# Kernel optimization log

Hardware: AMD Instinct MI355X
Metric: run time of the kernel (lower is better)

## Reference

```python
import jax, jax.numpy as jnp
import numpy as np

RADIUS = 1.0
BUMP = 32          # config.bump_steps
SCALE = 100.0      # sigmoid sharpness in compute_ecc
G = 32             # num_graphs

N, E, F = 16000, 48000, 32000
DIM, NDIR = 3, 64
HID, NC = 256, 10


def compute_ecc(h, index, lin):
    # h: [M, D]; lin: [BUMP] thresholds; index: [M] graph ids
    # sigmoid(scale * (lin - h)) broadcast -> [M, BUMP, D], segment-sum over M
    ecc = jax.nn.sigmoid(SCALE * (lin[None, :, None] - h[:, None, :]))
    return jax.ops.segment_sum(ecc, index, num_segments=G)  # [G, BUMP, D]


def setup_inputs() -> dict:
    key = jax.random.key(0)
    ks = jax.random.split(key, 12)
    x = jax.random.normal(ks[0], (N, DIM), dtype=jnp.float32)
    node_weights = jax.random.uniform(ks[1], (N,), dtype=jnp.float32)
    edge_weights = jax.random.uniform(ks[2], (E,), dtype=jnp.float32)
    face_weights = jax.random.uniform(ks[3], (F,), dtype=jnp.float32)
    v = jax.random.normal(ks[4], (DIM, NDIR), dtype=jnp.float32)
    v = v / jnp.linalg.norm(v, axis=0, keepdims=True)  # unit directions
    W1 = jax.random.normal(ks[5], (HID, NDIR * BUMP), dtype=jnp.float32) * 0.02
    b1 = jnp.zeros((HID,), dtype=jnp.float32)
    W2 = jax.random.normal(ks[6], (NC, HID), dtype=jnp.float32) * 0.02
    b2 = jnp.zeros((NC,), dtype=jnp.float32)
    edge_index = jax.random.randint(ks[7], (2, E), 0, N, dtype=jnp.int64)
    face = jax.random.randint(ks[8], (3, F), 0, N, dtype=jnp.int64)
    batch_ids = jnp.sort(jax.random.randint(ks[9], (N,), 0, G, dtype=jnp.int64))
    return {"x": x, "node_weights": node_weights, "edge_weights": edge_weights,
            "face_weights": face_weights, "v": v, "W1": W1, "b1": b1,
            "W2": W2, "b2": b2, "edge_index": edge_index, "face": face,
            "batch_ids": batch_ids}


def reference(x, node_weights, edge_weights, face_weights, v, W1, b1, W2, b2,
              edge_index, face, batch_ids):
    lin = jnp.linspace(-RADIUS, RADIUS, BUMP, dtype=jnp.float32)
    # node heights: weighted coords projected onto directions -> [N, D]
    nh = (x * node_weights[:, None]) @ v
    # edge heights: max over the 2 endpoints, then weight -> [E, D]
    eh = jnp.maximum(nh[edge_index[0]], nh[edge_index[1]]) * edge_weights[:, None]
    idx_e = batch_ids[edge_index[0]]
    # face heights: max over the 3 vertices -> [F, D]
    fh = jnp.max(nh[face], axis=0) * face_weights[:, None]
    idx_f = batch_ids[face[0]]
    ecc = compute_ecc(nh, batch_ids, lin)   # [G, BUMP, D]
    ecc = ecc - compute_ecc(eh, idx_e, lin)
    ecc = ecc + compute_ecc(fh, idx_f, lin)
    flat = ecc.reshape(G, -1)               # [G, BUMP*D]
    h = jax.nn.relu(flat @ W1.T + b1)
    logits = h @ W2.T + b2
    return (logits, flat)
```

## Files before the change

kernel.cpp:

```cpp
#include <hip/hip_runtime.h>
#include <hip/hip_bf16.h>

constexpr int NN = 16000, NE = 48000, NF = 32000;
constexpr int ND = 64, NB = 32, NG = 32;
constexpr int HIDN = 256, NCLS = 10;
constexpr int CHB = 32;
constexpr int EFB = (NE + NF + 255) / 256;
constexpr int PREB = (NN * ND) / 256;
constexpr int CAPE = 4096, CAPF = 4096;
constexpr float KLOG = 144.26950408889634f;
constexpr float DLT  = 9.307710457348151f;
constexpr float INV_DLT = 0.10743849569269015f;
constexpr int HBINS = 39;

constexpr int NH_OFF   = 0;
constexpr int ECCF_OFF = NH_OFF + NN * ND;
constexpr int CUR_OFF  = ECCF_OFF + NG * NB * ND;
constexpr int NOFS_OFF = CUR_OFF + 64;
constexpr int PE_OFF   = NOFS_OFF + 34;
constexpr int PF_OFF   = PE_OFF + NG * CAPE / 2;
constexpr int HB_OFF   = PF_OFF + NG * CAPF / 2;
constexpr int ZERO_CNT = NG * NB * ND;

__device__ __forceinline__ int clamp_node(int n) {
    return ((unsigned)n < (unsigned)NN) ? n : 0;
}
template<bool BF> __device__ __forceinline__ float ldf(const void* p, int i) {
    return BF ? __bfloat162float(((const __hip_bfloat16*)p)[i]) : ((const float*)p)[i];
}
template<bool I64> __device__ __forceinline__ int ldi(const int* p, int i) {
    return I64 ? p[2 * i] : p[i];
}

__device__ __forceinline__ bool detect_bf(const void* xp) {
    const unsigned* xw = (const unsigned*)xp;
    unsigned w = xw[threadIdx.x & 63];
    return __ballot(((w >> 23) & 0xFFu) >= 200u) != 0ull;
}
__device__ __forceinline__ bool detect_i64(const int* eip) {
    const unsigned* eiw = (const unsigned*)eip;
    unsigned o = eiw[2 * (threadIdx.x & 63) + 1];
    return __ballot(o != 0u) == 0ull;
}

__device__ __forceinline__ void accum_hist(float h, float s, float* hb) {
    const float KDEC = __builtin_amdgcn_exp2f(-DLT);
    float hkL = fmaf(h, KLOG, KLOG);
    float fl = floorf((hkL - 14.0f) * INV_DLT);
    int jlo = (int)fl + 1;
    if (jlo >= 32) return;
    if (jlo < -4) { hb[4 * 64] += s; return; }
    float t0 = fmaf(-(fl + 1.0f), DLT, hkL);
    float e  = __builtin_amdgcn_exp2f(t0);
    float s0 = __builtin_amdgcn_rcpf(1.0f + e);  e *= KDEC;
    float s1 = __builtin_amdgcn_rcpf(1.0f + e);  e *= KDEC;
    float s2 = __builtin_amdgcn_rcpf(1.0f + e);
    float* p = hb + (jlo + 4) * 64;
    float v0 = p[0], v1 = p[64], v2 = p[128], v3 = p[192];
    p[0]   = v0 + s * s0;
    p[64]  = v1 + s * (s1 - s0);
    p[128] = v2 + s * (s2 - s1);
    p[192] = v3 + s * (1.0f - s2);
}

template<bool BF, bool I64>
__device__ __forceinline__ void pre_body(const void* x, const void* nw, const void* v,
                                         const int* ei, const int* fc, const int* batch,
                                         float* wsf, int* wsi, unsigned* cur,
                                         unsigned short* pe, unsigned short* pf,
                                         unsigned* cnt, unsigned* base) {
    int t = threadIdx.x;
    int gid = blockIdx.x * 256 + t;

    if (gid < ZERO_CNT) wsf[ECCF_OFF + gid] = 0.0f;

    if (gid < NN) {
        int gn = ldi<I64>(batch, gid) & (NG - 1);
        int gp = (gid > 0) ? (ldi<I64>(batch, gid - 1) & (NG - 1)) : -1;
        for (int gg = gp + 1; gg <= gn; gg++) wsi[NOFS_OFF + gg] = gid;
        if (gid == NN - 1)
            for (int gg = gn + 1; gg <= NG; gg++) wsi[NOFS_OFF + gg] = NN;
    }

    {
        int n = gid >> 6, d = gid & 63;
        float h = fmaf(ldf<BF>(x, n*3+2), ldf<BF>(v, 2*ND+d),
                  fmaf(ldf<BF>(x, n*3+1), ldf<BF>(v, ND+d),
                       ldf<BF>(x, n*3+0) * ldf<BF>(v, d))) * ldf<BF>(nw, n);
        wsf[NH_OFF + gid] = h;
    }

    if (blockIdx.x < EFB) {
        if (t < 64) cnt[t] = 0;
        __syncthreads();
        int id = blockIdx.x * 256 + t;
        int bin = 0; unsigned rank = 0; bool act = false;
        if (id < NE + NF) {
            if (id < NE) bin = ldi<I64>(batch, clamp_node(ldi<I64>(ei, id))) & 31;
            else bin = 32 + (ldi<I64>(batch, clamp_node(ldi<I64>(fc, id - NE))) & 31);
            act = true;
            rank = atomicAdd(&cnt[bin], 1u);
        }
        __syncthreads();
        if (t < 64) base[t] = cnt[t] ? atomicAdd(&cur[t], cnt[t]) : 0u;
        __syncthreads();
        if (act) {
            int off = (int)(base[bin] + rank);
            if (bin < 32) { if (off < CAPE) pe[bin * CAPE + off] = (unsigned short)id; }
            else { if (off < CAPF) pf[(bin - 32) * CAPF + off] = (unsigned short)(id - NE); }
        }
    }
}
__global__ __launch_bounds__(256) void k_pre(const void* __restrict__ x,
                                             const void* __restrict__ nw,
                                             const void* __restrict__ v,
                                             const int* __restrict__ ei,
                                             const int* __restrict__ fc,
                                             const int* __restrict__ batch,
                                             float* __restrict__ wsf,
                                             int* __restrict__ wsi,
                                             unsigned* __restrict__ cur,
                                             unsigned short* __restrict__ pe,
                                             unsigned short* __restrict__ pf) {
    __shared__ unsigned cnt[64], base[64];
    bool bf = detect_bf(x), i64 = detect_i64(ei);
    if (bf)  { if (i64) pre_body<true,true >(x,nw,v,ei,fc,batch,wsf,wsi,cur,pe,pf,cnt,base);
               else     pre_body<true,false>(x,nw,v,ei,fc,batch,wsf,wsi,cur,pe,pf,cnt,base); }
    else     { if (i64) pre_body<false,true >(x,nw,v,ei,fc,batch,wsf,wsi,cur,pe,pf,cnt,base);
               else     pre_body<false,false>(x,nw,v,ei,fc,batch,wsf,wsi,cur,pe,pf,cnt,base); }
}

template<bool BF, bool I64>
__device__ __forceinline__ void ecc_body(const int* ei, const int* fc,
                                         const void* ew, const void* fw,
                                         const float* nh, const int* wsi,
                                         const unsigned* cur, float* eccf,
                                         const unsigned short* pe,
                                         const unsigned short* pf,
                                         float* hist) {
    int t = threadIdx.x;
    int d = t & 63;
    int w = __builtin_amdgcn_readfirstlane(t) >> 6;
    int g  = blockIdx.x >> 5;
    int cb = blockIdx.x & (CHB - 1);
    int sid = cb * 4 + w;
    const int S = CHB * 4;

    for (int j = t; j < 4 * HBINS * 64; j += 256) hist[j] = 0.0f;
    __syncthreads();

    float* hb = hist + w * (HBINS * 64) + d;

    int ns = wsi[NOFS_OFF + g], nend = wsi[NOFS_OFF + g + 1];
    int i = ns + sid;
    for (; i + 3 * S < nend; i += 4 * S) {
        float h1 = nh[i * ND + d];
        float h2 = nh[(i + S) * ND + d];
        float h3 = nh[(i + 2 * S) * ND + d];
        float h4 = nh[(i + 3 * S) * ND + d];
        accum_hist(h1, 1.0f, hb);
        accum_hist(h2, 1.0f, hb);
        accum_hist(h3, 1.0f, hb);
        accum_hist(h4, 1.0f, hb);
    }
    for (; i < nend; i += S) accum_hist(nh[i * ND + d], 1.0f, hb);

    int ecnt = min((int)cur[g], CAPE);
    i = sid;
    for (; i + 3 * S < ecnt; i += 4 * S) {
        int e1 = pe[g * CAPE + i];
        int e2 = pe[g * CAPE + i + S];
        int e3 = pe[g * CAPE + i + 2 * S];
        int e4 = pe[g * CAPE + i + 3 * S];
        int a1 = clamp_node(ldi<I64>(ei, e1)), b1 = clamp_node(ldi<I64>(ei, NE + e1));
        int a2 = clamp_node(ldi<I64>(ei, e2)), b2 = clamp_node(ldi<I64>(ei, NE + e2));
        int a3 = clamp_node(ldi<I64>(ei, e3)), b3 = clamp_node(ldi<I64>(ei, NE + e3));
        int a4 = clamp_node(ldi<I64>(ei, e4)), b4 = clamp_node(ldi<I64>(ei, NE + e4));
        float w1 = ldf<BF>(ew, e1), w2 = ldf<BF>(ew, e2);
        float w3 = ldf<BF>(ew, e3), w4 = ldf<BF>(ew, e4);
        float h1 = fmaxf(nh[a1 * ND + d], nh[b1 * ND + d]) * w1;
        float h2 = fmaxf(nh[a2 * ND + d], nh[b2 * ND + d]) * w2;
        float h3 = fmaxf(nh[a3 * ND + d], nh[b3 * ND + d]) * w3;
        float h4 = fmaxf(nh[a4 * ND + d], nh[b4 * ND + d]) * w4;
        accum_hist(h1, -1.0f, hb);
        accum_hist(h2, -1.0f, hb);
        accum_hist(h3, -1.0f, hb);
        accum_hist(h4, -1.0f, hb);
    }
    for (; i < ecnt; i += S) {
        int e = pe[g * CAPE + i];
        int a = clamp_node(ldi<I64>(ei, e)), b = clamp_node(ldi<I64>(ei, NE + e));
        accum_hist(fmaxf(nh[a * ND + d], nh[b * ND + d]) * ldf<BF>(ew, e), -1.0f, hb);
    }

    int fcnt = min((int)cur[32 + g], CAPF);
    i = sid;
    for (; i + 3 * S < fcnt; i += 4 * S) {
        int f1 = pf[g * CAPF + i];
        int f2 = pf[g * CAPF + i + S];
        int f3 = pf[g * CAPF + i + 2 * S];
        int f4 = pf[g * CAPF + i + 3 * S];
        int a1 = clamp_node(ldi<I64>(fc, f1)), b1 = clamp_node(ldi<I64>(fc, NF + f1));
        int c1 = clamp_node(ldi<I64>(fc, 2*NF + f1));
        int a2 = clamp_node(ldi<I64>(fc, f2)), b2 = clamp_node(ldi<I64>(fc, NF + f2));
        int c2 = clamp_node(ldi<I64>(fc, 2*NF + f2));
        int a3 = clamp_node(ldi<I64>(fc, f3)), b3 = clamp_node(ldi<I64>(fc, NF + f3));
        int c3 = clamp_node(ldi<I64>(fc, 2*NF + f3));
        int a4 = clamp_node(ldi<I64>(fc, f4)), b4 = clamp_node(ldi<I64>(fc, NF + f4));
        int c4 = clamp_node(ldi<I64>(fc, 2*NF + f4));
        float w1 = ldf<BF>(fw, f1), w2 = ldf<BF>(fw, f2);
        float w3 = ldf<BF>(fw, f3), w4 = ldf<BF>(fw, f4);
        float h1 = fmaxf(fmaxf(nh[a1*ND+d], nh[b1*ND+d]), nh[c1*ND+d]) * w1;
        float h2 = fmaxf(fmaxf(nh[a2*ND+d], nh[b2*ND+d]), nh[c2*ND+d]) * w2;
        float h3 = fmaxf(fmaxf(nh[a3*ND+d], nh[b3*ND+d]), nh[c3*ND+d]) * w3;
        float h4 = fmaxf(fmaxf(nh[a4*ND+d], nh[b4*ND+d]), nh[c4*ND+d]) * w4;
        accum_hist(h1, 1.0f, hb);
        accum_hist(h2, 1.0f, hb);
        accum_hist(h3, 1.0f, hb);
        accum_hist(h4, 1.0f, hb);
    }
    for (; i < fcnt; i += S) {
        int f = pf[g * CAPF + i];
        int a = clamp_node(ldi<I64>(fc, f)), b = clamp_node(ldi<I64>(fc, NF + f));
        int c = clamp_node(ldi<I64>(fc, 2*NF + f));
        accum_hist(fmaxf(fmaxf(nh[a*ND+d], nh[b*ND+d]), nh[c*ND+d]) * ldf<BF>(fw, f),
                   1.0f, hb);
    }

    __syncthreads();
    for (int o = t; o < HBINS * 64; o += 256)
        hist[o] += hist[HBINS*64 + o] + hist[2*HBINS*64 + o] + hist[3*HBINS*64 + o];
    __syncthreads();
    if (t < 64) {
        float run = hist[t] + hist[64 + t] + hist[128 + t] + hist[192 + t];
        float* eb = eccf + g * (NB * ND) + t;
        for (int j = 0; j < 32; j++) {
            run += hist[(j + 4) * 64 + t];
            atomicAdd(eb + j * 64, run);
        }
    }
}
__global__ __launch_bounds__(256, 4) void k_ecc(const int* __restrict__ ei,
                                                const int* __restrict__ fc,
                                                const void* __restrict__ ew,
                                                const void* __restrict__ fw,
                                                const float* __restrict__ nh,
                                                const int* __restrict__ wsi,
                                                const unsigned* __restrict__ cur,
                                                float* __restrict__ eccf,
                                                const unsigned short* __restrict__ pe,
                                                const unsigned short* __restrict__ pf,
                                                const void* __restrict__ x) {
    __shared__ float hist[4 * HBINS * 64];
    bool bf = detect_bf(x), i64 = detect_i64(ei);
    if (bf)  { if (i64) ecc_body<true,true >(ei,fc,ew,fw,nh,wsi,cur,eccf,pe,pf,hist);
               else     ecc_body<true,false>(ei,fc,ew,fw,nh,wsi,cur,eccf,pe,pf,hist); }
    else     { if (i64) ecc_body<false,true >(ei,fc,ew,fw,nh,wsi,cur,eccf,pe,pf,hist);
               else     ecc_body<false,false>(ei,fc,ew,fw,nh,wsi,cur,eccf,pe,pf,hist); }
}

template<bool BF>
__device__ __forceinline__ void mlp1_body(const void* W1, const void* b1,
                                          const float* eccf, float* hbuf,
                                          void* outv, float* red, float* pr) {
    int g = blockIdx.x >> 3, hc = blockIdx.x & 7;
    int t = threadIdx.x;

    const float4* fp = (const float4*)(eccf + g * (NB * ND) + t * 8);
    float4 fa = fp[0], fb = fp[1];
    float fl[8] = {fa.x, fa.y, fa.z, fa.w, fb.x, fb.y, fb.z, fb.w};

    if (hc == 0) {
        int ob = NG * NCLS + g * (NB * ND) + t * 8;
        if (BF) {
#pragma unroll
            for (int j = 0; j < 8; j++)
                ((__hip_bfloat16*)outv)[ob + j] = __float2bfloat16(fl[j]);
        } else {
            ((float4*)((float*)outv + ob))[0] = fa;
            ((float4*)((float*)outv + ob))[1] = fb;
        }
    }

    float acc[32];
#pragma unroll
    for (int r = 0; r < 32; r++) acc[r] = 0.0f;
#pragma unroll 4
    for (int r = 0; r < 32; r++) {
        size_t wb = (size_t)(hc * 32 + r) * (NB * ND) + t * 8;
        float wv[8];
        if (BF) {
            uint4 u = *(const uint4*)((const __hip_bfloat16*)W1 + wb);
            wv[0] = __uint_as_float(u.x << 16); wv[1] = __uint_as_float(u.x & 0xffff0000u);
            wv[2] = __uint_as_float(u.y << 16); wv[3] = __uint_as_float(u.y & 0xffff0000u);
            wv[4] = __uint_as_float(u.z << 16); wv[5] = __uint_as_float(u.z & 0xffff0000u);
            wv[6] = __uint_as_float(u.w << 16); wv[7] = __uint_as_float(u.w & 0xffff0000u);
        } else {
            float4 a = *(const float4*)((const float*)W1 + wb);
            float4 b = *(const float4*)((const float*)W1 + wb + 4);
            wv[0]=a.x; wv[1]=a.y; wv[2]=a.z; wv[3]=a.w;
            wv[4]=b.x; wv[5]=b.y; wv[6]=b.z; wv[7]=b.w;
        }
        float s = 0.0f;
#pragma unroll
        for (int j = 0; j < 8; j++) s = fmaf(wv[j], fl[j], s);
        acc[r] = s;
    }

#pragma unroll
    for (int r = 0; r < 32; r++) red[t * 33 + r] = acc[r];
    __syncthreads();
    {
        int r = t >> 3, s8 = t & 7;
        float sum = 0.0f;
#pragma unroll
        for (int i = 0; i < 32; i++) sum += red[(s8 * 32 + i) * 33 + r];
        pr[r * 8 + s8] = sum;
    }
    __syncthreads();
    if (t < 32) {
        float h = ldf<BF>(b1, hc * 32 + t);
#pragma unroll
        for (int s8 = 0; s8 < 8; s8++) h += pr[t * 8 + s8];
        hbuf[g * HIDN + hc * 32 + t] = fmaxf(h, 0.0f);
    }
}
__global__ __launch_bounds__(256) void k_mlp1(const void* __restrict__ W1,
                                              const void* __restrict__ b1,
                                              const float* __restrict__ eccf,
                                              float* __restrict__ hbuf,
                                              void* __restrict__ outv,
                                              const void* __restrict__ x) {
    __shared__ float red[256 * 33];
    __shared__ float pr[256];
    if (detect_bf(x)) mlp1_body<true>(W1, b1, eccf, hbuf, outv, red, pr);
    else              mlp1_body<false>(W1, b1, eccf, hbuf, outv, red, pr);
}

template<bool BF>
__device__ __forceinline__ void mlp2_body(const void* W2, const void* b2,
                                          const float* hbuf, void* outv, float* hs) {
    int g = blockIdx.x, t = threadIdx.x;
    hs[t] = hbuf[g * HIDN + t];
    __syncthreads();
    int w = t >> 6, lane = t & 63;
    for (int c = w; c < NCLS; c += 4) {
        float p = hs[lane]        * ldf<BF>(W2, c * HIDN + lane)
                + hs[lane + 64]   * ldf<BF>(W2, c * HIDN + lane + 64)
                + hs[lane + 128]  * ldf<BF>(W2, c * HIDN + lane + 128)
                + hs[lane + 192]  * ldf<BF>(W2, c * HIDN + lane + 192);
#pragma unroll
        for (int off = 32; off >= 1; off >>= 1) p += __shfl_xor(p, off);
        if (lane == 0) {
            float r = p + ldf<BF>(b2, c);
            if (BF) ((__hip_bfloat16*)outv)[g * NCLS + c] = __float2bfloat16(r);
            else    ((float*)outv)[g * NCLS + c] = r;
        }
    }
}
__global__ __launch_bounds__(256) void k_mlp2(const void* __restrict__ W2,
                                              const void* __restrict__ b2,
                                              const float* __restrict__ hbuf,
                                              void* __restrict__ outv,
                                              const void* __restrict__ x) {
    __shared__ float hs[HIDN];
    if (detect_bf(x)) mlp2_body<true>(W2, b2, hbuf, outv, hs);
    else              mlp2_body<false>(W2, b2, hbuf, outv, hs);
}

extern "C" void kernel_launch(void* const* d_in, const int* in_sizes, int n_in,
                              void* d_out, int out_size, void* d_ws, size_t ws_size,
                              hipStream_t stream) {
    const void* x  = d_in[0];
    const void* nw = d_in[1];
    const void* ew = d_in[2];
    const void* fw = d_in[3];
    const void* v  = d_in[4];
    const void* W1 = d_in[5];
    const void* b1 = d_in[6];
    const void* W2 = d_in[7];
    const void* b2 = d_in[8];
    const int* ei    = (const int*)d_in[9];
    const int* fc    = (const int*)d_in[10];
    const int* batch = (const int*)d_in[11];

    float*    wsf = (float*)d_ws;
    unsigned* wsu = (unsigned*)d_ws;
    int*      wsi = (int*)d_ws;
    float*    nh   = wsf + NH_OFF;
    float*    eccf = wsf + ECCF_OFF;
    unsigned* cur  = wsu + CUR_OFF;
    float*    hbuf = wsf + HB_OFF;
    unsigned short* pe = (unsigned short*)(wsi + PE_OFF);
    unsigned short* pf = (unsigned short*)(wsi + PF_OFF);

    hipMemsetAsync((char*)d_ws + (size_t)CUR_OFF * 4, 0, 64 * 4, stream);

    k_pre<<<PREB, 256, 0, stream>>>(x, nw, v, ei, fc, batch, wsf, wsi, cur, pe, pf);
    k_ecc<<<NG * CHB, 256, 0, stream>>>(ei, fc, ew, fw, nh, wsi, cur, eccf, pe, pf, x);
    k_mlp1<<<NG * 8, 256, 0, stream>>>(W1, b1, eccf, hbuf, d_out, x);
    k_mlp2<<<NG, 256, 0, stream>>>(W2, b2, hbuf, d_out, x);
}
```

Before: 124.5 us.

## Pack edge/face endpoints and weights into records during bucketing, prefetch in ecc

The bucketing pass now writes compact per-graph records holding packed endpoint indices and the weight, instead of 16-bit edge/face ids. The ECC kernel then reads one record per edge or face rather than chasing ids into the edge_index, face and weight arrays, which removes one level of dependent gathers. The unrolled loops also software-prefetch the next batch of records while the current node heights are being loaded. The cost is larger workspace records and extra gathers in the pre kernel. The 14-bit index packing holds because node ids are below 16384.

Result: faster. 121.1 us (-2.7%).

```diff
diff --git a/kernel.cpp b/kernel.cpp
--- a/kernel.cpp
+++ b/kernel.cpp
@@ -13,13 +13,16 @@
 constexpr float INV_DLT = 0.10743849569269015f;
 constexpr int HBINS = 39;
 
+struct alignas(8)  ERec { unsigned ab; float w; };
+struct alignas(16) FRec { unsigned ab; unsigned c; float w; unsigned pad; };
+
 constexpr int NH_OFF   = 0;
 constexpr int ECCF_OFF = NH_OFF + NN * ND;
 constexpr int CUR_OFF  = ECCF_OFF + NG * NB * ND;
 constexpr int NOFS_OFF = CUR_OFF + 64;
-constexpr int PE_OFF   = NOFS_OFF + 34;
-constexpr int PF_OFF   = PE_OFF + NG * CAPE / 2;
-constexpr int HB_OFF   = PF_OFF + NG * CAPF / 2;
+constexpr int ER_OFF   = NOFS_OFF + 36;
+constexpr int FR_OFF   = ER_OFF + NG * CAPE * 2;
+constexpr int HB_OFF   = FR_OFF + NG * CAPF * 4;
 constexpr int ZERO_CNT = NG * NB * ND;
 
 __device__ __forceinline__ int clamp_node(int n) {
@@ -66,8 +69,9 @@
 template<bool BF, bool I64>
 __device__ __forceinline__ void pre_body(const void* x, const void* nw, const void* v,
                                          const int* ei, const int* fc, const int* batch,
+                                         const void* ew, const void* fw,
                                          float* wsf, int* wsi, unsigned* cur,
-                                         unsigned short* pe, unsigned short* pf,
+                                         ERec* er, FRec* fr,
                                          unsigned* cnt, unsigned* base) {
     int t = threadIdx.x;
     int gid = blockIdx.x * 256 + t;
@@ -106,8 +110,24 @@
         __syncthreads();
         if (act) {
             int off = (int)(base[bin] + rank);
-            if (bin < 32) { if (off < CAPE) pe[bin * CAPE + off] = (unsigned short)id; }
-            else { if (off < CAPF) pf[(bin - 32) * CAPF + off] = (unsigned short)(id - NE); }
+            if (bin < 32) {
+                if (off < CAPE) {
+                    unsigned a = (unsigned)clamp_node(ldi<I64>(ei, id));
+                    unsigned b = (unsigned)clamp_node(ldi<I64>(ei, NE + id));
+                    ERec r; r.ab = a | (b << 14); r.w = ldf<BF>(ew, id);
+                    er[bin * CAPE + off] = r;
+                }
+            } else {
+                if (off < CAPF) {
+                    int fid = id - NE;
+                    unsigned a = (unsigned)clamp_node(ldi<I64>(fc, fid));
+                    unsigned b = (unsigned)clamp_node(ldi<I64>(fc, NF + fid));
+                    unsigned c = (unsigned)clamp_node(ldi<I64>(fc, 2 * NF + fid));
+                    FRec r; r.ab = a | (b << 14); r.c = c;
+                    r.w = ldf<BF>(fw, fid); r.pad = 0u;
+                    fr[(bin - 32) * CAPF + off] = r;
+                }
+            }
         }
     }
 }
@@ -117,27 +137,28 @@
                                              const int* __restrict__ ei,
                                              const int* __restrict__ fc,
                                              const int* __restrict__ batch,
+                                             const void* __restrict__ ew,
+                                             const void* __restrict__ fw,
                                              float* __restrict__ wsf,
                                              int* __restrict__ wsi,
                                              unsigned* __restrict__ cur,
-                                             unsigned short* __restrict__ pe,
-                                             unsigned short* __restrict__ pf) {
+                                             ERec* __restrict__ er,
+                                             FRec* __restrict__ fr) {
     __shared__ unsigned cnt[64], base[64];
     bool bf = detect_bf(x), i64 = detect_i64(ei);
-    if (bf)  { if (i64) pre_body<true,true >(x,nw,v,ei,fc,batch,wsf,wsi,cur,pe,pf,cnt,base);
-               else     pre_body<true,false>(x,nw,v,ei,fc,batch,wsf,wsi,cur,pe,pf,cnt,base); }
-    else     { if (i64) pre_body<false,true >(x,nw,v,ei,fc,batch,wsf,wsi,cur,pe,pf,cnt,base);
-               else     pre_body<false,false>(x,nw,v,ei,fc,batch,wsf,wsi,cur,pe,pf,cnt,base); }
-}
-
-template<bool BF, bool I64>
-__device__ __forceinline__ void ecc_body(const int* ei, const int* fc,
-                                         const void* ew, const void* fw,
-                                         const float* nh, const int* wsi,
-                                         const unsigned* cur, float* eccf,
-                                         const unsigned short* pe,
-                                         const unsigned short* pf,
-                                         float* hist) {
+    if (bf)  { if (i64) pre_body<true,true >(x,nw,v,ei,fc,batch,ew,fw,wsf,wsi,cur,er,fr,cnt,base);
+               else     pre_body<true,false>(x,nw,v,ei,fc,batch,ew,fw,wsf,wsi,cur,er,fr,cnt,base); }
+    else     { if (i64) pre_body<false,true >(x,nw,v,ei,fc,batch,ew,fw,wsf,wsi,cur,er,fr,cnt,base);
+               else     pre_body<false,false>(x,nw,v,ei,fc,batch,ew,fw,wsf,wsi,cur,er,fr,cnt,base); }
+}
+
+__global__ __launch_bounds__(256, 4) void k_ecc(const float* __restrict__ nh,
+                                                const int* __restrict__ wsi,
+                                                const unsigned* __restrict__ cur,
+                                                float* __restrict__ eccf,
+                                                const ERec* __restrict__ er,
+                                                const FRec* __restrict__ fr) {
+    __shared__ float hist[4 * HBINS * 64];
     int t = threadIdx.x;
     int d = t & 63;
     int w = __builtin_amdgcn_readfirstlane(t) >> 6;
@@ -166,65 +187,66 @@
     for (; i < nend; i += S) accum_hist(nh[i * ND + d], 1.0f, hb);
 
     int ecnt = min((int)cur[g], CAPE);
+    const ERec* eg = er + g * CAPE;
     i = sid;
-    for (; i + 3 * S < ecnt; i += 4 * S) {
-        int e1 = pe[g * CAPE + i];
-        int e2 = pe[g * CAPE + i + S];
-        int e3 = pe[g * CAPE + i + 2 * S];
-        int e4 = pe[g * CAPE + i + 3 * S];
-        int a1 = clamp_node(ldi<I64>(ei, e1)), b1 = clamp_node(ldi<I64>(ei, NE + e1));
-        int a2 = clamp_node(ldi<I64>(ei, e2)), b2 = clamp_node(ldi<I64>(ei, NE + e2));
-        int a3 = clamp_node(ldi<I64>(ei, e3)), b3 = clamp_node(ldi<I64>(ei, NE + e3));
-        int a4 = clamp_node(ldi<I64>(ei, e4)), b4 = clamp_node(ldi<I64>(ei, NE + e4));
-        float w1 = ldf<BF>(ew, e1), w2 = ldf<BF>(ew, e2);
-        float w3 = ldf<BF>(ew, e3), w4 = ldf<BF>(ew, e4);
-        float h1 = fmaxf(nh[a1 * ND + d], nh[b1 * ND + d]) * w1;
-        float h2 = fmaxf(nh[a2 * ND + d], nh[b2 * ND + d]) * w2;
-        float h3 = fmaxf(nh[a3 * ND + d], nh[b3 * ND + d]) * w3;
-        float h4 = fmaxf(nh[a4 * ND + d], nh[b4 * ND + d]) * w4;
-        accum_hist(h1, -1.0f, hb);
-        accum_hist(h2, -1.0f, hb);
-        accum_hist(h3, -1.0f, hb);
-        accum_hist(h4, -1.0f, hb);
+    if (i + 3 * S < ecnt) {
+        ERec r1 = eg[i], r2 = eg[i + S], r3 = eg[i + 2 * S], r4 = eg[i + 3 * S];
+        for (;;) {
+            int ni = i + 4 * S;
+            bool more = (ni + 3 * S < ecnt);
+            float a1 = nh[(r1.ab & 16383) * ND + d], b1 = nh[((r1.ab >> 14) & 16383) * ND + d];
+            float a2 = nh[(r2.ab & 16383) * ND + d], b2 = nh[((r2.ab >> 14) & 16383) * ND + d];
+            float a3 = nh[(r3.ab & 16383) * ND + d], b3 = nh[((r3.ab >> 14) & 16383) * ND + d];
+            float a4 = nh[(r4.ab & 16383) * ND + d], b4 = nh[((r4.ab >> 14) & 16383) * ND + d];
+            ERec n1, n2, n3, n4;
+            if (more) { n1 = eg[ni]; n2 = eg[ni + S]; n3 = eg[ni + 2 * S]; n4 = eg[ni + 3 * S]; }
+            accum_hist(fmaxf(a1, b1) * r1.w, -1.0f, hb);
+            accum_hist(fmaxf(a2, b2) * r2.w, -1.0f, hb);
+            accum_hist(fmaxf(a3, b3) * r3.w, -1.0f, hb);
+            accum_hist(fmaxf(a4, b4) * r4.w, -1.0f, hb);
+            i = ni;
+            if (!more) break;
+            r1 = n1; r2 = n2; r3 = n3; r4 = n4;
+        }
     }
     for (; i < ecnt; i += S) {
-        int e = pe[g * CAPE + i];
-        int a = clamp_node(ldi<I64>(ei, e)), b = clamp_node(ldi<I64>(ei, NE + e));
-        accum_hist(fmaxf(nh[a * ND + d], nh[b * ND + d]) * ldf<BF>(ew, e), -1.0f, hb);
+        ERec r = eg[i];
+        float ha = nh[(r.ab & 16383) * ND + d], hbv = nh[((r.ab >> 14) & 16383) * ND + d];
+        accum_hist(fmaxf(ha, hbv) * r.w, -1.0f, hb);
     }
 
     int fcnt = min((int)cur[32 + g], CAPF);
+    const FRec* fg = fr + g * CAPF;
     i = sid;
-    for (; i + 3 * S < fcnt; i += 4 * S) {
-        int f1 = pf[g * CAPF + i];
-        int f2 = pf[g * CAPF + i + S];
-        int f3 = pf[g * CAPF + i + 2 * S];
-        int f4 = pf[g * CAPF + i + 3 * S];
-        int a1 = clamp_node(ldi<I64>(fc, f1)), b1 = clamp_node(ldi<I64>(fc, NF + f1));
-        int c1 = clamp_node(ldi<I64>(fc, 2*NF + f1));
-        int a2 = clamp_node(ldi<I64>(fc, f2)), b2 = clamp_node(ldi<I64>(fc, NF + f2));
-        int c2 = clamp_node(ldi<I64>(fc, 2*NF + f2));
-        int a3 = clamp_node(ldi<I64>(fc, f3)), b3 = clamp_node(ldi<I64>(fc, NF + f3));
-        int c3 = clamp_node(ldi<I64>(fc, 2*NF + f3));
-        int a4 = clamp_node(ldi<I64>(fc, f4)), b4 = clamp_node(ldi<I64>(fc, NF + f4));
-        int c4 = clamp_node(ldi<I64>(fc, 2*NF + f4));
-        float w1 = ldf<BF>(fw, f1), w2 = ldf<BF>(fw, f2);
-        float w3 = ldf<BF>(fw, f3), w4 = ldf<BF>(fw, f4);
-        float h1 = fmaxf(fmaxf(nh[a1*ND+d], nh[b1*ND+d]), nh[c1*ND+d]) * w1;
-        float h2 = fmaxf(fmaxf(nh[a2*ND+d], nh[b2*ND+d]), nh[c2*ND+d]) * w2;
-        float h3 = fmaxf(fmaxf(nh[a3*ND+d], nh[b3*ND+d]), nh[c3*ND+d]) * w3;
-        float h4 = fmaxf(fmaxf(nh[a4*ND+d], nh[b4*ND+d]), nh[c4*ND+d]) * w4;
-        accum_hist(h1, 1.0f, hb);
-        accum_hist(h2, 1.0f, hb);
-        accum_hist(h3, 1.0f, hb);
-        accum_hist(h4, 1.0f, hb);
+    if (i + 3 * S < fcnt) {
+        FRec r1 = fg[i], r2 = fg[i + S], r3 = fg[i + 2 * S], r4 = fg[i + 3 * S];
+        for (;;) {
+            int ni = i + 4 * S;
+            bool more = (ni + 3 * S < fcnt);
+            float a1 = nh[(r1.ab & 16383) * ND + d], b1 = nh[((r1.ab >> 14) & 16383) * ND + d];
+            float c1 = nh[r1.c * ND + d];
+            float a2 = nh[(r2.ab & 16383) * ND + d], b2 = nh[((r2.ab >> 14) & 16383) * ND + d];
+            float c2 = nh[r2.c * ND + d];
+            float a3 = nh[(r3.ab & 16383) * ND + d], b3 = nh[((r3.ab >> 14) & 16383) * ND + d];
+            float c3 = nh[r3.c * ND + d];
+            float a4 = nh[(r4.ab & 16383) * ND + d], b4 = nh[((r4.ab >> 14) & 16383) * ND + d];
+            float c4 = nh[r4.c * ND + d];
+            FRec n1, n2, n3, n4;
+            if (more) { n1 = fg[ni]; n2 = fg[ni + S]; n3 = fg[ni + 2 * S]; n4 = fg[ni + 3 * S]; }
+            accum_hist(fmaxf(fmaxf(a1, b1), c1) * r1.w, 1.0f, hb);
+            accum_hist(fmaxf(fmaxf(a2, b2), c2) * r2.w, 1.0f, hb);
+            accum_hist(fmaxf(fmaxf(a3, b3), c3) * r3.w, 1.0f, hb);
+            accum_hist(fmaxf(fmaxf(a4, b4), c4) * r4.w, 1.0f, hb);
+            i = ni;
+            if (!more) break;
+            r1 = n1; r2 = n2; r3 = n3; r4 = n4;
+        }
     }
     for (; i < fcnt; i += S) {
-        int f = pf[g * CAPF + i];
-        int a = clamp_node(ldi<I64>(fc, f)), b = clamp_node(ldi<I64>(fc, NF + f));
-        int c = clamp_node(ldi<I64>(fc, 2*NF + f));
-        accum_hist(fmaxf(fmaxf(nh[a*ND+d], nh[b*ND+d]), nh[c*ND+d]) * ldf<BF>(fw, f),
-                   1.0f, hb);
+        FRec r = fg[i];
+        float ha = nh[(r.ab & 16383) * ND + d], hbv = nh[((r.ab >> 14) & 16383) * ND + d];
+        float hc = nh[r.c * ND + d];
+        accum_hist(fmaxf(fmaxf(ha, hbv), hc) * r.w, 1.0f, hb);
     }
 
     __syncthreads();
@@ -239,24 +261,6 @@
             atomicAdd(eb + j * 64, run);
         }
     }
-}
-__global__ __launch_bounds__(256, 4) void k_ecc(const int* __restrict__ ei,
-                                                const int* __restrict__ fc,
-                                                const void* __restrict__ ew,
-                                                const void* __restrict__ fw,
-                                                const float* __restrict__ nh,
-                                                const int* __restrict__ wsi,
-                                                const unsigned* __restrict__ cur,
-                                                float* __restrict__ eccf,
-                                                const unsigned short* __restrict__ pe,
-                                                const unsigned short* __restrict__ pf,
-                                                const void* __restrict__ x) {
-    __shared__ float hist[4 * HBINS * 64];
-    bool bf = detect_bf(x), i64 = detect_i64(ei);
-    if (bf)  { if (i64) ecc_body<true,true >(ei,fc,ew,fw,nh,wsi,cur,eccf,pe,pf,hist);
-               else     ecc_body<true,false>(ei,fc,ew,fw,nh,wsi,cur,eccf,pe,pf,hist); }
-    else     { if (i64) ecc_body<false,true >(ei,fc,ew,fw,nh,wsi,cur,eccf,pe,pf,hist);
-               else     ecc_body<false,false>(ei,fc,ew,fw,nh,wsi,cur,eccf,pe,pf,hist); }
 }
 
 template<bool BF>
@@ -391,13 +395,13 @@
     float*    eccf = wsf + ECCF_OFF;
     unsigned* cur  = wsu + CUR_OFF;
     float*    hbuf = wsf + HB_OFF;
-    unsigned short* pe = (unsigned short*)(wsi + PE_OFF);
-    unsigned short* pf = (unsigned short*)(wsi + PF_OFF);
+    ERec*     er   = (ERec*)(wsf + ER_OFF);
+    FRec*     fr   = (FRec*)(wsf + FR_OFF);
 
     hipMemsetAsync((char*)d_ws + (size_t)CUR_OFF * 4, 0, 64 * 4, stream);
 
-    k_pre<<<PREB, 256, 0, stream>>>(x, nw, v, ei, fc, batch, wsf, wsi, cur, pe, pf);
-    k_ecc<<<NG * CHB, 256, 0, stream>>>(ei, fc, ew, fw, nh, wsi, cur, eccf, pe, pf, x);
+    k_pre<<<PREB, 256, 0, stream>>>(x, nw, v, ei, fc, batch, ew, fw, wsf, wsi, cur, er, fr);
+    k_ecc<<<NG * CHB, 256, 0, stream>>>(nh, wsi, cur, eccf, er, fr);
     k_mlp1<<<NG * 8, 256, 0, stream>>>(W1, b1, eccf, hbuf, d_out, x);
     k_mlp2<<<NG, 256, 0, stream>>>(W2, b2, hbuf, d_out, x);
 }
```
